# Kernel optimization log

Measured on AMD Instinct MI355X. Metric: run time of the kernel, lower is better.

## Reference

```python
import jax, jax.numpy as jnp
import numpy as np

N, DIN = 8192, 768
DH1, DO1 = 64, 64
DH2, DO2 = 32, 64


def setup_inputs() -> dict:
    key = jax.random.key(0)
    ks = jax.random.split(key, 12)
    s = lambda *sh: 0.02
    inp = {
        "X": jax.random.normal(ks[0], (N, DIN), jnp.float32),
        "A": jax.random.randint(ks[1], (N, N), 0, 2, jnp.int32),
        # GAT layer 1: W (din->dh), a (2dh), W2 (dh->dout) + bias
        "W1": jax.random.normal(ks[2], (DIN, DH1), jnp.float32) * 0.02,
        "a1": jax.random.normal(ks[3], (2 * DH1,), jnp.float32) * 0.02,
        "W21": jax.random.normal(ks[4], (DH1, DO1), jnp.float32) * 0.02,
        "b21": jnp.zeros((DO1,), jnp.float32),
        # GAT layer 2
        "Wg2": jax.random.normal(ks[5], (DO1, DH2), jnp.float32) * 0.02,
        "a2": jax.random.normal(ks[6], (2 * DH2,), jnp.float32) * 0.02,
        "W22": jax.random.normal(ks[7], (DH2, DO2), jnp.float32) * 0.02,
        "b22": jnp.zeros((DO2,), jnp.float32),
        # MLP head: 64 -> 64 -> 2
        "M1": jax.random.normal(ks[8], (DO2, 64), jnp.float32) * 0.02,
        "bm1": jnp.zeros((64,), jnp.float32),
        "M2": jax.random.normal(ks[9], (64, 2), jnp.float32) * 0.02,
        "bm2": jnp.zeros((2,), jnp.float32),
    }
    return inp


def _tiny_gat(X, A, W, a, W2, b2):
    # H = X @ W; e_ij = a . [H_i, H_j] = H_i@a_src + H_j@a_dst (same math,
    # no N x N x 2dh intermediate)
    H = X @ W                      # [N, dh]
    dh = W.shape[1]
    e = (H @ a[:dh])[:, None] + (H @ a[dh:])[None, :]   # [N, N]
    e = jnp.where(A == 0, jnp.float32(-1e9), e)
    alpha = jax.nn.softmax(e, axis=1)                   # softmax over neighbors j
    Z = alpha @ H                                       # [N, dh]
    return jax.nn.elu(Z @ W2 + b2)


def reference(X, A, W1, a1, W21, b21, Wg2, a2, W22, b22, M1, bm1, M2, bm2):
    Z = _tiny_gat(X, A, W1, a1, W21, b21)    # [N, 64]
    Z = _tiny_gat(Z, A, Wg2, a2, W22, b22)   # [N, 64]
    g = Z.mean(axis=0)                       # [64]
    h = jax.nn.relu(g @ M1 + bm1)
    return h @ M2 + bm2                      # [2]
```

## Files before the change

### kernel.cpp

```cpp
#include <hip/hip_runtime.h>


#define NN 8192

typedef __attribute__((ext_vector_type(8))) short s16x8;
typedef __attribute__((ext_vector_type(4))) float f32x4;
union V16 { uint4 u; s16x8 s; };

static constexpr size_t OFF_WBITS = 0;
static constexpr size_t OFF_GT1H  = (size_t)8 << 20;
static constexpr size_t OFF_GT1L  = (size_t)9 << 20;
static constexpr size_t OFF_U1    = (size_t)10 << 20;
static constexpr size_t OFF_DEN1  = ((size_t)10 << 20) + 32 * 1024;
static constexpr size_t OFF_GT2H  = ((size_t)10 << 20) + 128 * 1024;
static constexpr size_t OFF_GT2L  = ((size_t)10 << 20) + 896 * 1024;
static constexpr size_t OFF_GPART = ((size_t)11 << 20) + 768 * 1024;
static constexpr size_t OFF_NUMP  = (size_t)12 << 20;
static constexpr size_t OFF_DP    = (size_t)45 << 20;

__device__ __forceinline__ float elu_f(float x) {
    return x > 0.f ? x : expm1f(x);
}
__device__ __forceinline__ unsigned int bf16_rne(float x) {
    unsigned int u = __float_as_uint(x);
    return (u + 0x7FFFu + ((u >> 16) & 1u)) >> 16;
}
__device__ __forceinline__ unsigned int split_pack(float g) {
    unsigned int hi = bf16_rne(g);
    float fhi = __uint_as_float(hi << 16);
    unsigned int lo = bf16_rne(g - fhi);
    return (hi << 16) | lo;
}
__device__ __forceinline__ void split3(float f, unsigned int& h, unsigned int& m,
                                       unsigned int& l) {
    h = bf16_rne(f);
    float fh = __uint_as_float(h << 16);
    float r1 = f - fh;
    m = bf16_rne(r1);
    float fm = __uint_as_float(m << 16);
    l = bf16_rne(r1 - fm);
}
__device__ __forceinline__ unsigned int bits2bf(unsigned int b2) {
    return (b2 & 1u) * 0x3F80u + (b2 & 2u) * 0x1FC00000u;
}

__global__ __launch_bounds__(256) void k_xw1m(const float* __restrict__ X,
                                              const float* __restrict__ W1,
                                              float* __restrict__ Dp) {
    __shared__ unsigned int fh[6144];
    __shared__ unsigned int fl[6144];
    const int tid = threadIdx.x, wv = tid >> 6, lane = tid & 63;
    const int ks = blockIdx.y;
    for (int i = tid; i < 6144; i += 256) {
        const int feat = i & 63, kp = i >> 6;
        const int kg = ks * 192 + 2 * kp;
        float w0 = W1[(size_t)kg * 64 + feat];
        float w1 = W1[(size_t)(kg + 1) * 64 + feat];
        unsigned int h0 = bf16_rne(w0);
        unsigned int l0 = bf16_rne(w0 - __uint_as_float(h0 << 16));
        unsigned int h1 = bf16_rne(w1);
        unsigned int l1 = bf16_rne(w1 - __uint_as_float(h1 << 16));
        const int mt = feat >> 4, n = feat & 15;
        const int ktl = kp >> 4, rem = kp & 15, quad = rem >> 2, q = rem & 3;
        const int idx = ((mt * 6 + ktl) * 64 + quad * 16 + n) * 4 + q;
        fh[idx] = h0 | (h1 << 16);
        fl[idx] = l0 | (l1 << 16);
    }
    __syncthreads();
    const int n = lane & 15, quad = lane >> 4;
    const int node = blockIdx.x * 64 + wv * 16 + n;
    const int ntg = blockIdx.x * 4 + wv;
    f32x4 acc[4];
#pragma unroll
    for (int mt = 0; mt < 4; ++mt) acc[mt] = (f32x4){0.f, 0.f, 0.f, 0.f};
    const float4* X4 = (const float4*)X;
    for (int kk = 0; kk < 6; ++kk) {
        const int ktg = ks * 6 + kk;
        float4 x01 = X4[(size_t)node * 192 + ktg * 8 + quad * 2];
        float4 x23 = X4[(size_t)node * 192 + ktg * 8 + quad * 2 + 1];
        float xf[8] = {x01.x, x01.y, x01.z, x01.w, x23.x, x23.y, x23.z, x23.w};
        V16 bh, bm, bl;
        unsigned int* bhp = (unsigned int*)&bh.u;
        unsigned int* bmp = (unsigned int*)&bm.u;
        unsigned int* blp = (unsigned int*)&bl.u;
#pragma unroll
        for (int q = 0; q < 4; ++q) {
            unsigned int h0, m0, l0, h1, m1, l1;
            split3(xf[2 * q], h0, m0, l0);
            split3(xf[2 * q + 1], h1, m1, l1);
            bhp[q] = h0 | (h1 << 16);
            bmp[q] = m0 | (m1 << 16);
            blp[q] = l0 | (l1 << 16);
        }
#pragma unroll
        for (int mt = 0; mt < 4; ++mt) {
            const int base = ((mt * 6 + kk) * 64 + lane) * 4;
            V16 awh, awl;
            awh.u = *(const uint4*)&fh[base];
            awl.u = *(const uint4*)&fl[base];
            acc[mt] = __builtin_amdgcn_mfma_f32_16x16x32_bf16(awh.s, bh.s, acc[mt], 0, 0, 0);
            acc[mt] = __builtin_amdgcn_mfma_f32_16x16x32_bf16(awh.s, bm.s, acc[mt], 0, 0, 0);
            acc[mt] = __builtin_amdgcn_mfma_f32_16x16x32_bf16(awh.s, bl.s, acc[mt], 0, 0, 0);
            acc[mt] = __builtin_amdgcn_mfma_f32_16x16x32_bf16(awl.s, bh.s, acc[mt], 0, 0, 0);
            acc[mt] = __builtin_amdgcn_mfma_f32_16x16x32_bf16(awl.s, bm.s, acc[mt], 0, 0, 0);
        }
    }
#pragma unroll
    for (int mt = 0; mt < 4; ++mt)
        *(f32x4*)&Dp[(size_t)(((ks * 4 + mt) * 512 + ntg) * 64 + lane) * 4] = acc[mt];
}

__global__ __launch_bounds__(256) void k_xcomb(const float* __restrict__ Dp,
                                               const float* __restrict__ a1,
                                               unsigned int* __restrict__ Gt1h,
                                               unsigned int* __restrict__ Gt1l,
                                               float* __restrict__ u1) {
    __shared__ float Hsh[64][33];
    __shared__ float us[32];
    const int tid = threadIdx.x;
    if (tid < 128) {
        const int ntl = tid >> 6, lane = tid & 63;
        const int n = lane & 15, quad = lane >> 4;
        const int ntg = blockIdx.x * 2 + ntl;
        float dpart = 0.f;
#pragma unroll
        for (int mt = 0; mt < 4; ++mt) {
            float v[4] = {0.f, 0.f, 0.f, 0.f};
#pragma unroll
            for (int ksp = 0; ksp < 4; ++ksp) {
                const float* p = &Dp[(size_t)(((ksp * 4 + mt) * 512 + ntg) * 64 + lane) * 4];
                v[0] += p[0]; v[1] += p[1]; v[2] += p[2]; v[3] += p[3];
            }
#pragma unroll
            for (int r = 0; r < 4; ++r) {
                int feat = mt * 16 + quad * 4 + r;
                Hsh[feat][ntl * 16 + n] = v[r];
                dpart += v[r] * a1[64 + feat];
            }
        }
        dpart += __shfl_xor(dpart, 16);
        dpart += __shfl_xor(dpart, 32);
        float uu = expf(dpart);
        if (lane < 16) {
            us[ntl * 16 + lane] = uu;
            u1[blockIdx.x * 32 + ntl * 16 + lane] = uu;
        }
    }
    __syncthreads();
    {
        const int mt = tid >> 6, lane = tid & 63;
        const int feat = mt * 16 + (lane & 15), quad = lane >> 4;
        uint4 hv, lv;
        unsigned int g0, g1;
#define PACK_Q(Q, FX)                                                   \
        {                                                               \
            int j0 = quad * 8 + 2 * Q;                                  \
            g0 = split_pack(us[j0] * Hsh[feat][j0]);                    \
            g1 = split_pack(us[j0 + 1] * Hsh[feat][j0 + 1]);            \
            hv.FX = (g0 >> 16) | (g1 & 0xFFFF0000u);                    \
            lv.FX = (g0 & 0xFFFFu) | (g1 << 16);                        \
        }
        PACK_Q(0, x) PACK_Q(1, y) PACK_Q(2, z) PACK_Q(3, w)
#undef PACK_Q
        size_t base = ((size_t)(mt * 256 + blockIdx.x) * 64 + lane) * 4;
        *(uint4*)(Gt1h + base) = hv;
        *(uint4*)(Gt1l + base) = lv;
    }
}

__global__ __launch_bounds__(256) void k_pack(const int* __restrict__ A,
                                              const float* __restrict__ u1,
                                              unsigned int* __restrict__ Wb32,
                                              float* __restrict__ den1) {
    __shared__ unsigned short msh[4][512];
    const int tid = threadIdx.x, wv = tid >> 6, lane = tid & 63;
    const int row0 = blockIdx.x * 4;
    const int row = row0 + wv;
    float dsum = 0.f;
    for (int c = 0; c < 8; ++c) {
        const int j = c * 1024 + lane * 16;
        const int4* A0 = (const int4*)(A + (size_t)row * NN + j);
        const float4* U4 = (const float4*)(u1 + j);
        int4 a0 = A0[0], a1 = A0[1], a2 = A0[2], a3 = A0[3];
        float4 u0 = U4[0], u4 = U4[1], u8 = U4[2], uc = U4[3];
        unsigned int m0 = 0;
#define DO4(AV, UV, SH)                                                \
        m0 |= ((AV.x != 0) << (SH)) | ((AV.y != 0) << (SH + 1)) |      \
              ((AV.z != 0) << (SH + 2)) | ((AV.w != 0) << (SH + 3));   \
        dsum += (AV.x != 0 ? UV.x : 0.f) + (AV.y != 0 ? UV.y : 0.f) +  \
                (AV.z != 0 ? UV.z : 0.f) + (AV.w != 0 ? UV.w : 0.f);
        DO4(a0, u0, 0) DO4(a1, u4, 4) DO4(a2, u8, 8) DO4(a3, uc, 12)
#undef DO4
        msh[wv][c * 64 + lane] = (unsigned short)m0;
    }
#pragma unroll
    for (int off = 32; off; off >>= 1) dsum += __shfl_down(dsum, off);
    if (lane == 0) den1[row] = dsum;
    __syncthreads();
    {
        const int r = tid >> 6, i = tid & 63;
        const uint4* src = (const uint4*)&msh[r][0];
        uint4* dst = (uint4*)(Wb32 + (size_t)(row0 + r) * 256);
        dst[i] = src[i];
    }
}

__global__ __launch_bounds__(256) void k_attn1(const unsigned int* __restrict__ Wb32,
                                               const unsigned int* __restrict__ Gt1h,
                                               const unsigned int* __restrict__ Gt1l,
                                               float* __restrict__ num1p) {
    __shared__ unsigned int bw[64 * 36];
    const int tid = threadIdx.x, wv = tid >> 6, lane = tid & 63;
    const int node0 = blockIdx.x * 64;
    const int kt0 = blockIdx.y * 32;
    {
        const int r = tid >> 2, part = tid & 3;
        const uint4* src = (const uint4*)(Wb32 + (size_t)(node0 + r) * 256 + kt0 + part * 8);
        uint4 v0 = src[0], v1 = src[1];
        *(uint4*)&bw[r * 36 + part * 8] = v0;
        *(uint4*)&bw[r * 36 + part * 8 + 4] = v1;
    }
    __syncthreads();
    const int n = lane & 15, quad = lane >> 4;
    const int mt = wv;
    f32x4 acc[4];
#pragma unroll
    for (int nt = 0; nt < 4; ++nt) acc[nt] = (f32x4){0.f, 0.f, 0.f, 0.f};
#pragma unroll 4
    for (int ks = 0; ks < 32; ++ks) {
        size_t base = ((size_t)(mt * 256 + kt0 + ks) * 64 + lane) * 4;
        V16 ah, al;
        ah.u = *(const uint4*)(Gt1h + base);
        al.u = *(const uint4*)(Gt1l + base);
#pragma unroll
        for (int nt = 0; nt < 4; ++nt) {
            unsigned int by8 = (bw[(nt * 16 + n) * 36 + ks] >> (quad * 8)) & 0xFFu;
            V16 bf;
            bf.u = make_uint4(bits2bf(by8), bits2bf(by8 >> 2),
                              bits2bf(by8 >> 4), bits2bf(by8 >> 6));
            acc[nt] = __builtin_amdgcn_mfma_f32_16x16x32_bf16(ah.s, bf.s, acc[nt], 0, 0, 0);
            acc[nt] = __builtin_amdgcn_mfma_f32_16x16x32_bf16(al.s, bf.s, acc[nt], 0, 0, 0);
        }
    }
    const int s = blockIdx.y;
#pragma unroll
    for (int nt = 0; nt < 4; ++nt) {
        const int node = node0 + nt * 16 + n;
        *(f32x4*)&num1p[((size_t)s * NN + node) * 64 + mt * 16 + quad * 4] = acc[nt];
    }
}

__global__ __launch_bounds__(256) void k_ep1(const float* __restrict__ num1p,
                                             const float* __restrict__ den1,
                                             const float* __restrict__ W21,
                                             const float* __restrict__ b21,
                                             const float* __restrict__ Wg2,
                                             const float* __restrict__ a2,
                                             unsigned int* __restrict__ Gt2h,
                                             unsigned int* __restrict__ Gt2l) {
    __shared__ float w21sh[64 * 64];
    __shared__ float wg2sh[64 * 32];
    __shared__ float zsh[4][64];
    __shared__ float osh[4][64];
    __shared__ unsigned int g2sh[32][9];
    __shared__ unsigned int u2sh[8];
    const int tid = threadIdx.x, wv = tid >> 6, lane = tid & 63;
    const int node0 = blockIdx.x * 8;
    {
        const float4* s4 = (const float4*)W21;
        float4* d4 = (float4*)w21sh;
        d4[tid] = s4[tid];
        d4[tid + 256] = s4[tid + 256];
        d4[tid + 512] = s4[tid + 512];
        d4[tid + 768] = s4[tid + 768];
        ((float4*)wg2sh)[tid] = ((const float4*)Wg2)[tid];
        ((float4*)wg2sh)[tid + 256] = ((const float4*)Wg2)[tid + 256];
    }
    const float bb = b21[lane];
    const int l32 = lane & 31;
    const float a2v = (lane < 32) ? a2[32 + l32] : 0.f;
    __syncthreads();
    for (int it = 0; it < 2; ++it) {
        const int node = node0 + wv * 2 + it;
        float sacc = 0.f;
#pragma unroll
        for (int sp = 0; sp < 8; ++sp)
            sacc += num1p[((size_t)sp * NN + node) * 64 + lane];
        zsh[wv][lane] = sacc / den1[node];
        __builtin_amdgcn_wave_barrier();
        const float4* zv = (const float4*)&zsh[wv][0];
        float o0 = 0.f, o1 = 0.f;
#pragma unroll 4
        for (int c4 = 0; c4 < 16; ++c4) {
            float4 z4 = zv[c4];
            const int c = c4 * 4;
            o0 += z4.x * w21sh[(c + 0) * 64 + lane] + z4.y * w21sh[(c + 1) * 64 + lane];
            o1 += z4.z * w21sh[(c + 2) * 64 + lane] + z4.w * w21sh[(c + 3) * 64 + lane];
        }
        float o = elu_f(bb + o0 + o1);
        osh[wv][lane] = o;
        __builtin_amdgcn_wave_barrier();
        const float4* ov = (const float4*)&osh[wv][0];
        float h0 = 0.f, h1 = 0.f;
#pragma unroll 4
        for (int c4 = 0; c4 < 16; ++c4) {
            float4 o4 = ov[c4];
            const int c = c4 * 4;
            h0 += o4.x * wg2sh[(c + 0) * 32 + l32] + o4.y * wg2sh[(c + 1) * 32 + l32];
            h1 += o4.z * wg2sh[(c + 2) * 32 + l32] + o4.w * wg2sh[(c + 3) * 32 + l32];
        }
        float hval = h0 + h1;
        float pp = hval * a2v;
#pragma unroll
        for (int off = 32; off; off >>= 1) pp += __shfl_down(pp, off);
        float d2 = __shfl(pp, 0);
        float uu = expf(d2);
        const int nodeloc = wv * 2 + it;
        if (lane == 0) u2sh[nodeloc] = split_pack(uu);
        if (lane < 32) g2sh[l32][nodeloc] = split_pack(uu * hval);
    }
    __syncthreads();
    if (tid < 48) {
        const int mt = tid >> 4, ml = tid & 15;
        const int quad_w = blockIdx.x & 3, kt = blockIdx.x >> 2;
        const int lane2 = quad_w * 16 + ml;
        uint4 hv, lv;
        unsigned int g0, g1;
#define PACK_Q(Q, F)                                                   \
        {                                                              \
            int j0 = 2 * Q;                                            \
            if (mt < 2) { g0 = g2sh[mt * 16 + ml][j0];                 \
                          g1 = g2sh[mt * 16 + ml][j0 + 1]; }           \
            else if (ml == 0) { g0 = u2sh[j0]; g1 = u2sh[j0 + 1]; }    \
            else { g0 = 0; g1 = 0; }                                   \
            hv.F = (g0 >> 16) | (g1 & 0xFFFF0000u);                    \
            lv.F = (g0 & 0xFFFFu) | (g1 << 16);                        \
        }
        PACK_Q(0, x) PACK_Q(1, y) PACK_Q(2, z) PACK_Q(3, w)
#undef PACK_Q
        size_t base = ((size_t)(mt * 256 + kt) * 64 + lane2) * 4;
        *(uint4*)(Gt2h + base) = hv;
        *(uint4*)(Gt2l + base) = lv;
    }
}

__global__ __launch_bounds__(256) void k_attn2(const unsigned int* __restrict__ Wb32,
                                               const unsigned int* __restrict__ Gt2h,
                                               const unsigned int* __restrict__ Gt2l,
                                               float* __restrict__ num2p) {
    __shared__ unsigned int bw[64 * 36];
    const int tid = threadIdx.x, wv = tid >> 6, lane = tid & 63;
    const int node0 = blockIdx.x * 64;
    const int kt0 = blockIdx.y * 32;
    {
        const int r = tid >> 2, part = tid & 3;
        const uint4* src = (const uint4*)(Wb32 + (size_t)(node0 + r) * 256 + kt0 + part * 8);
        uint4 v0 = src[0], v1 = src[1];
        *(uint4*)&bw[r * 36 + part * 8] = v0;
        *(uint4*)&bw[r * 36 + part * 8 + 4] = v1;
    }
    __syncthreads();
    if (wv == 3) return;
    const int n = lane & 15, quad = lane >> 4;
    const int mt = wv;
    f32x4 acc[4];
#pragma unroll
    for (int nt = 0; nt < 4; ++nt) acc[nt] = (f32x4){0.f, 0.f, 0.f, 0.f};
#pragma unroll 4
    for (int ks = 0; ks < 32; ++ks) {
        size_t base = ((size_t)(mt * 256 + kt0 + ks) * 64 + lane) * 4;
        V16 ah, al;
        ah.u = *(const uint4*)(Gt2h + base);
        al.u = *(const uint4*)(Gt2l + base);
#pragma unroll
        for (int nt = 0; nt < 4; ++nt) {
            unsigned int by8 = (bw[(nt * 16 + n) * 36 + ks] >> (quad * 8)) & 0xFFu;
            V16 bf;
            bf.u = make_uint4(bits2bf(by8), bits2bf(by8 >> 2),
                              bits2bf(by8 >> 4), bits2bf(by8 >> 6));
            acc[nt] = __builtin_amdgcn_mfma_f32_16x16x32_bf16(ah.s, bf.s, acc[nt], 0, 0, 0);
            acc[nt] = __builtin_amdgcn_mfma_f32_16x16x32_bf16(al.s, bf.s, acc[nt], 0, 0, 0);
        }
    }
    const int s = blockIdx.y;
#pragma unroll
    for (int nt = 0; nt < 4; ++nt) {
        const int node = node0 + nt * 16 + n;
        *(f32x4*)&num2p[((size_t)s * NN + node) * 48 + mt * 16 + quad * 4] = acc[nt];
    }
}

__global__ __launch_bounds__(512) void k_ep2(const float* __restrict__ num2p,
                                             const float* __restrict__ W22,
                                             const float* __restrict__ b22,
                                             float* __restrict__ gpart) {
    __shared__ float w22sh[32 * 64];
    __shared__ float zsh[8][32];
    __shared__ float gsh[8][64];
    const int tid = threadIdx.x, wv = tid >> 6, lane = tid & 63;
    ((float4*)w22sh)[tid] = ((const float4*)W22)[tid];
    const float bb = b22[lane];
    __syncthreads();
    float greg = 0.f;
    for (int it = 0; it < 4; ++it) {
        const int row = blockIdx.x * 32 + wv * 4 + it;
        float val = 0.f;
        if (lane < 33) {
#pragma unroll
            for (int sp = 0; sp < 8; ++sp)
                val += num2p[((size_t)sp * NN + row) * 48 + lane];
        }
        float den = __shfl(val, 32);
        if (lane < 32) zsh[wv][lane] = val / den;
        __builtin_amdgcn_wave_barrier();
        const float4* zv = (const float4*)&zsh[wv][0];
        float o0 = 0.f, o1 = 0.f;
#pragma unroll 4
        for (int c4 = 0; c4 < 8; ++c4) {
            float4 z4 = zv[c4];
            const int c = c4 * 4;
            o0 += z4.x * w22sh[(c + 0) * 64 + lane] + z4.y * w22sh[(c + 1) * 64 + lane];
            o1 += z4.z * w22sh[(c + 2) * 64 + lane] + z4.w * w22sh[(c + 3) * 64 + lane];
        }
        greg += elu_f(bb + o0 + o1);
        __builtin_amdgcn_wave_barrier();
    }
    gsh[wv][lane] = greg;
    __syncthreads();
    if (tid < 64) {
        float s = 0.f;
#pragma unroll
        for (int w = 0; w < 8; ++w) s += gsh[w][tid];
        gpart[(size_t)blockIdx.x * 64 + tid] = s;
    }
}

__global__ __launch_bounds__(256) void k_head(const float* __restrict__ gpart,
                                              const float* __restrict__ M1,
                                              const float* __restrict__ bm1,
                                              const float* __restrict__ M2,
                                              const float* __restrict__ bm2,
                                              float* __restrict__ outp) {
    __shared__ float part[4][64];
    __shared__ float gsh[64];
    __shared__ float hsh[64];
    const int tid = threadIdx.x, col = tid & 63, p = tid >> 6;
    float s = 0.f;
    for (int b = p * 64; b < p * 64 + 64; ++b)
        s += gpart[(size_t)b * 64 + col];
    part[p][col] = s;
    __syncthreads();
    if (tid < 64)
        gsh[tid] = (part[0][tid] + part[1][tid] + part[2][tid] + part[3][tid])
                   * (1.0f / 8192.0f);
    __syncthreads();
    if (tid < 64) {
        float h = bm1[tid];
        for (int c = 0; c < 64; ++c) h += gsh[c] * M1[c * 64 + tid];
        hsh[tid] = h > 0.f ? h : 0.f;
    }
    __syncthreads();
    if (tid < 2) {
        float o = bm2[tid];
        for (int j = 0; j < 64; ++j) o += hsh[j] * M2[j * 2 + tid];
        outp[tid] = o;
    }
}

extern "C" void kernel_launch(void* const* d_in, const int* in_sizes, int n_in,
                              void* d_out, int out_size, void* d_ws, size_t ws_size,
                              hipStream_t stream) {
    const float* X   = (const float*)d_in[0];
    const int*   A   = (const int*)  d_in[1];
    const float* W1  = (const float*)d_in[2];
    const float* a1  = (const float*)d_in[3];
    const float* W21 = (const float*)d_in[4];
    const float* b21 = (const float*)d_in[5];
    const float* Wg2 = (const float*)d_in[6];
    const float* a2  = (const float*)d_in[7];
    const float* W22 = (const float*)d_in[8];
    const float* b22 = (const float*)d_in[9];
    const float* M1  = (const float*)d_in[10];
    const float* bm1 = (const float*)d_in[11];
    const float* M2  = (const float*)d_in[12];
    const float* bm2 = (const float*)d_in[13];
    float* out = (float*)d_out;

    char* ws = (char*)d_ws;
    unsigned int* Wbits = (unsigned int*)(ws + OFF_WBITS);
    unsigned int* Gt1h  = (unsigned int*)(ws + OFF_GT1H);
    unsigned int* Gt1l  = (unsigned int*)(ws + OFF_GT1L);
    unsigned int* Gt2h  = (unsigned int*)(ws + OFF_GT2H);
    unsigned int* Gt2l  = (unsigned int*)(ws + OFF_GT2L);
    float* Dp    = (float*)(ws + OFF_DP);
    float* u1    = (float*)(ws + OFF_U1);
    float* den1  = (float*)(ws + OFF_DEN1);
    float* gpart = (float*)(ws + OFF_GPART);
    float* nump  = (float*)(ws + OFF_NUMP);

    k_xw1m <<<dim3(128, 4), 256, 0, stream>>>(X, W1, Dp);
    k_xcomb<<<256, 256, 0, stream>>>(Dp, a1, Gt1h, Gt1l, u1);
    k_pack <<<2048, 256, 0, stream>>>(A, u1, Wbits, den1);
    k_attn1<<<dim3(128, 8), 256, 0, stream>>>(Wbits, Gt1h, Gt1l, nump);
    k_ep1  <<<1024, 256, 0, stream>>>(nump, den1, W21, b21, Wg2, a2, Gt2h, Gt2l);
    k_attn2<<<dim3(128, 8), 256, 0, stream>>>(Wbits, Gt2h, Gt2l, nump);
    k_ep2  <<<256, 512, 0, stream>>>(nump, W22, b22, gpart);
    k_head <<<1, 256, 0, stream>>>(gpart, M1, bm1, M2, bm2, out);
}
```

Before: 519.5 us.

## Fuse adjacency bit-packing into attention-1 and fold softmax denominator into MFMA

Removes the separate k_pack kernel. k_attn1f now reads the int32 adjacency rows directly, packs them into bitmasks in shared memory, writes Wbits for later use by layer 2, and runs the attention MFMA in the same kernel. The denominator is computed by appending the exp-score vector u as an extra 'feature' tile (a fifth wave, 320 threads), so num1p gets an 80-wide stride with the denominator at column 64. This saves a kernel launch and one pass over Wbits, at the cost of a heavier attention kernel that now streams the 256MB adjacency itself.

```diff
diff --git a/kernel.cpp b/kernel.cpp
--- a/kernel.cpp
+++ b/kernel.cpp
@@ -9,14 +9,12 @@
 
 static constexpr size_t OFF_WBITS = 0;
 static constexpr size_t OFF_GT1H  = (size_t)8 << 20;
-static constexpr size_t OFF_GT1L  = (size_t)9 << 20;
-static constexpr size_t OFF_U1    = (size_t)10 << 20;
-static constexpr size_t OFF_DEN1  = ((size_t)10 << 20) + 32 * 1024;
-static constexpr size_t OFF_GT2H  = ((size_t)10 << 20) + 128 * 1024;
-static constexpr size_t OFF_GT2L  = ((size_t)10 << 20) + 896 * 1024;
-static constexpr size_t OFF_GPART = ((size_t)11 << 20) + 768 * 1024;
-static constexpr size_t OFF_NUMP  = (size_t)12 << 20;
-static constexpr size_t OFF_DP    = (size_t)45 << 20;
+static constexpr size_t OFF_GT1L  = ((size_t)9 << 20) + 512 * 1024;
+static constexpr size_t OFF_GT2H  = (size_t)11 << 20;
+static constexpr size_t OFF_GT2L  = (size_t)12 << 20;
+static constexpr size_t OFF_GPART = (size_t)13 << 20;
+static constexpr size_t OFF_NUMP  = (size_t)16 << 20;
+static constexpr size_t OFF_DP    = (size_t)40 << 20;
 
 __device__ __forceinline__ float elu_f(float x) {
     return x > 0.f ? x : expm1f(x);
@@ -113,8 +111,7 @@
 __global__ __launch_bounds__(256) void k_xcomb(const float* __restrict__ Dp,
                                                const float* __restrict__ a1,
                                                unsigned int* __restrict__ Gt1h,
-                                               unsigned int* __restrict__ Gt1l,
-                                               float* __restrict__ u1) {
+                                               unsigned int* __restrict__ Gt1l) {
     __shared__ float Hsh[64][33];
     __shared__ float us[32];
     const int tid = threadIdx.x;
@@ -141,10 +138,7 @@
         dpart += __shfl_xor(dpart, 16);
         dpart += __shfl_xor(dpart, 32);
         float uu = expf(dpart);
-        if (lane < 16) {
-            us[ntl * 16 + lane] = uu;
-            u1[blockIdx.x * 32 + ntl * 16 + lane] = uu;
-        }
+        if (lane < 16) us[ntl * 16 + lane] = uu;
     }
     __syncthreads();
     {
@@ -166,63 +160,68 @@
         *(uint4*)(Gt1h + base) = hv;
         *(uint4*)(Gt1l + base) = lv;
     }
-}
-
-__global__ __launch_bounds__(256) void k_pack(const int* __restrict__ A,
-                                              const float* __restrict__ u1,
-                                              unsigned int* __restrict__ Wb32,
-                                              float* __restrict__ den1) {
-    __shared__ unsigned short msh[4][512];
-    const int tid = threadIdx.x, wv = tid >> 6, lane = tid & 63;
-    const int row0 = blockIdx.x * 4;
-    const int row = row0 + wv;
-    float dsum = 0.f;
-    for (int c = 0; c < 8; ++c) {
-        const int j = c * 1024 + lane * 16;
-        const int4* A0 = (const int4*)(A + (size_t)row * NN + j);
-        const float4* U4 = (const float4*)(u1 + j);
-        int4 a0 = A0[0], a1 = A0[1], a2 = A0[2], a3 = A0[3];
-        float4 u0 = U4[0], u4 = U4[1], u8 = U4[2], uc = U4[3];
-        unsigned int m0 = 0;
-#define DO4(AV, UV, SH)                                                \
-        m0 |= ((AV.x != 0) << (SH)) | ((AV.y != 0) << (SH + 1)) |      \
-              ((AV.z != 0) << (SH + 2)) | ((AV.w != 0) << (SH + 3));   \
-        dsum += (AV.x != 0 ? UV.x : 0.f) + (AV.y != 0 ? UV.y : 0.f) +  \
-                (AV.z != 0 ? UV.z : 0.f) + (AV.w != 0 ? UV.w : 0.f);
-        DO4(a0, u0, 0) DO4(a1, u4, 4) DO4(a2, u8, 8) DO4(a3, uc, 12)
-#undef DO4
-        msh[wv][c * 64 + lane] = (unsigned short)m0;
-    }
-#pragma unroll
-    for (int off = 32; off; off >>= 1) dsum += __shfl_down(dsum, off);
-    if (lane == 0) den1[row] = dsum;
-    __syncthreads();
-    {
-        const int r = tid >> 6, i = tid & 63;
-        const uint4* src = (const uint4*)&msh[r][0];
-        uint4* dst = (uint4*)(Wb32 + (size_t)(row0 + r) * 256);
-        dst[i] = src[i];
-    }
-}
-
-__global__ __launch_bounds__(256) void k_attn1(const unsigned int* __restrict__ Wb32,
-                                               const unsigned int* __restrict__ Gt1h,
-                                               const unsigned int* __restrict__ Gt1l,
-                                               float* __restrict__ num1p) {
-    __shared__ unsigned int bw[64 * 36];
+    if (tid < 64) {
+        const int ml = tid & 15, quad = tid >> 4;
+        uint4 hv, lv;
+        unsigned int g0, g1;
+#define PACK_Q(Q, FX)                                                   \
+        {                                                               \
+            int j0 = quad * 8 + 2 * Q;                                  \
+            if (ml == 0) { g0 = split_pack(us[j0]);                     \
+                           g1 = split_pack(us[j0 + 1]); }               \
+            else { g0 = 0; g1 = 0; }                                    \
+            hv.FX = (g0 >> 16) | (g1 & 0xFFFF0000u);                    \
+            lv.FX = (g0 & 0xFFFFu) | (g1 << 16);                        \
+        }
+        PACK_Q(0, x) PACK_Q(1, y) PACK_Q(2, z) PACK_Q(3, w)
+#undef PACK_Q
+        size_t base = ((size_t)(4 * 256 + blockIdx.x) * 64 + tid) * 4;
+        *(uint4*)(Gt1h + base) = hv;
+        *(uint4*)(Gt1l + base) = lv;
+    }
+}
+
+__global__ __launch_bounds__(320) void k_attn1f(const int* __restrict__ A,
+                                                const unsigned int* __restrict__ Gt1h,
+                                                const unsigned int* __restrict__ Gt1l,
+                                                unsigned int* __restrict__ Wb32,
+                                                float* __restrict__ num1p) {
+    __shared__ unsigned int bw[64 * 33];
     const int tid = threadIdx.x, wv = tid >> 6, lane = tid & 63;
     const int node0 = blockIdx.x * 64;
-    const int kt0 = blockIdx.y * 32;
-    {
+    const int kc = blockIdx.y;
+    if (wv < 4) {
+        unsigned short* msh = (unsigned short*)bw;
+        for (int rr = 0; rr < 16; ++rr) {
+            const int r = wv * 16 + rr;
+            const int4* A4 = (const int4*)(A + (size_t)(node0 + r) * NN + kc * 1024 + lane * 16);
+            int4 a0 = A4[0], a1 = A4[1], a2 = A4[2], a3 = A4[3];
+            unsigned int m0 = 0;
+            m0 |= ((a0.x != 0) << 0)  | ((a0.y != 0) << 1)  |
+                  ((a0.z != 0) << 2)  | ((a0.w != 0) << 3);
+            m0 |= ((a1.x != 0) << 4)  | ((a1.y != 0) << 5)  |
+                  ((a1.z != 0) << 6)  | ((a1.w != 0) << 7);
+            m0 |= ((a2.x != 0) << 8)  | ((a2.y != 0) << 9)  |
+                  ((a2.z != 0) << 10) | ((a2.w != 0) << 11);
+            m0 |= ((a3.x != 0) << 12) | ((a3.y != 0) << 13) |
+                  ((a3.z != 0) << 14) | ((a3.w != 0) << 15);
+            msh[r * 66 + lane] = (unsigned short)m0;
+        }
+    }
+    __syncthreads();
+    if (tid < 256) {
         const int r = tid >> 2, part = tid & 3;
-        const uint4* src = (const uint4*)(Wb32 + (size_t)(node0 + r) * 256 + kt0 + part * 8);
-        uint4 v0 = src[0], v1 = src[1];
-        *(uint4*)&bw[r * 36 + part * 8] = v0;
-        *(uint4*)&bw[r * 36 + part * 8 + 4] = v1;
-    }
-    __syncthreads();
+        uint4 v0, v1;
+        v0.x = bw[r * 33 + part * 8 + 0]; v0.y = bw[r * 33 + part * 8 + 1];
+        v0.z = bw[r * 33 + part * 8 + 2]; v0.w = bw[r * 33 + part * 8 + 3];
+        v1.x = bw[r * 33 + part * 8 + 4]; v1.y = bw[r * 33 + part * 8 + 5];
+        v1.z = bw[r * 33 + part * 8 + 6]; v1.w = bw[r * 33 + part * 8 + 7];
+        uint4* dst = (uint4*)(Wb32 + (size_t)(node0 + r) * 256 + kc * 32 + part * 8);
+        dst[0] = v0; dst[1] = v1;
+    }
     const int n = lane & 15, quad = lane >> 4;
     const int mt = wv;
+    const int kt0 = kc * 32;
     f32x4 acc[4];
 #pragma unroll
     for (int nt = 0; nt < 4; ++nt) acc[nt] = (f32x4){0.f, 0.f, 0.f, 0.f};
@@ -234,7 +233,7 @@
         al.u = *(const uint4*)(Gt1l + base);
 #pragma unroll
         for (int nt = 0; nt < 4; ++nt) {
-            unsigned int by8 = (bw[(nt * 16 + n) * 36 + ks] >> (quad * 8)) & 0xFFu;
+            unsigned int by8 = (bw[(nt * 16 + n) * 33 + ks] >> (quad * 8)) & 0xFFu;
             V16 bf;
             bf.u = make_uint4(bits2bf(by8), bits2bf(by8 >> 2),
                               bits2bf(by8 >> 4), bits2bf(by8 >> 6));
@@ -246,12 +245,11 @@
 #pragma unroll
     for (int nt = 0; nt < 4; ++nt) {
         const int node = node0 + nt * 16 + n;
-        *(f32x4*)&num1p[((size_t)s * NN + node) * 64 + mt * 16 + quad * 4] = acc[nt];
+        *(f32x4*)&num1p[((size_t)s * NN + node) * 80 + mt * 16 + quad * 4] = acc[nt];
     }
 }
 
 __global__ __launch_bounds__(256) void k_ep1(const float* __restrict__ num1p,
-                                             const float* __restrict__ den1,
                                              const float* __restrict__ W21,
                                              const float* __restrict__ b21,
                                              const float* __restrict__ Wg2,
@@ -282,11 +280,14 @@
     __syncthreads();
     for (int it = 0; it < 2; ++it) {
         const int node = node0 + wv * 2 + it;
-        float sacc = 0.f;
-#pragma unroll
-        for (int sp = 0; sp < 8; ++sp)
-            sacc += num1p[((size_t)sp * NN + node) * 64 + lane];
-        zsh[wv][lane] = sacc / den1[node];
+        float sacc = 0.f, dnum = 0.f;
+#pragma unroll
+        for (int sp = 0; sp < 8; ++sp) {
+            const float* base = &num1p[((size_t)sp * NN + node) * 80];
+            sacc += base[lane];
+            dnum += base[64];
+        }
+        zsh[wv][lane] = sacc / dnum;
         __builtin_amdgcn_wave_barrier();
         const float4* zv = (const float4*)&zsh[wv][0];
         float o0 = 0.f, o1 = 0.f;
@@ -493,17 +494,14 @@
     unsigned int* Gt2h  = (unsigned int*)(ws + OFF_GT2H);
     unsigned int* Gt2l  = (unsigned int*)(ws + OFF_GT2L);
     float* Dp    = (float*)(ws + OFF_DP);
-    float* u1    = (float*)(ws + OFF_U1);
-    float* den1  = (float*)(ws + OFF_DEN1);
     float* gpart = (float*)(ws + OFF_GPART);
     float* nump  = (float*)(ws + OFF_NUMP);
 
-    k_xw1m <<<dim3(128, 4), 256, 0, stream>>>(X, W1, Dp);
-    k_xcomb<<<256, 256, 0, stream>>>(Dp, a1, Gt1h, Gt1l, u1);
-    k_pack <<<2048, 256, 0, stream>>>(A, u1, Wbits, den1);
-    k_attn1<<<dim3(128, 8), 256, 0, stream>>>(Wbits, Gt1h, Gt1l, nump);
-    k_ep1  <<<1024, 256, 0, stream>>>(nump, den1, W21, b21, Wg2, a2, Gt2h, Gt2l);
-    k_attn2<<<dim3(128, 8), 256, 0, stream>>>(Wbits, Gt2h, Gt2l, nump);
-    k_ep2  <<<256, 512, 0, stream>>>(nump, W22, b22, gpart);
-    k_head <<<1, 256, 0, stream>>>(gpart, M1, bm1, M2, bm2, out);
-}
+    k_xw1m  <<<dim3(128, 4), 256, 0, stream>>>(X, W1, Dp);
+    k_xcomb <<<256, 256, 0, stream>>>(Dp, a1, Gt1h, Gt1l);
+    k_attn1f<<<dim3(128, 8), 320, 0, stream>>>(A, Gt1h, Gt1l, Wbits, nump);
+    k_ep1   <<<1024, 256, 0, stream>>>(nump, W21, b21, Wg2, a2, Gt2h, Gt2l);
+    k_attn2 <<<dim3(128, 8), 256, 0, stream>>>(Wbits, Gt2h, Gt2l, nump);
+    k_ep2   <<<256, 512, 0, stream>>>(nump, W22, b22, gpart);
+    k_head  <<<1, 256, 0, stream>>>(gpart, M1, bm1, M2, bm2, out);
+}
```

After: 507.3 us. 2.3% less time.
